# Performance work log

Hardware: AMD Instinct MI355X
Metric: run time of the kernel (lower is better)

Reference implementation:

```python
import jax, jax.numpy as jnp
import numpy as np

V, K, D, T, B, M = 32000, 32, 256, 128, 128, 16
NEG = -1e9


def setup_inputs():
    key = jax.random.key(0)
    ks = jax.random.split(key, 32)
    def rn(k, shape):
        return (0.05 * jax.random.normal(k, shape)).astype(jnp.float32)
    u = jax.random.uniform(ks[4], (T, B, K), minval=1e-6, maxval=1.0 - 1e-6)
    return dict(
        keys=jax.random.randint(ks[0], (B, M), 1, V),
        vals=jax.random.randint(ks[1], (B, M), 1, V),
        sentences=jax.random.randint(ks[2], (B, T), 1, V),
        sent_lens=jax.random.randint(ks[3], (B,), T // 2, T + 1),
        tau=jnp.float32(0.5),
        x_lambd=jnp.float32(0.5),
        gumbel_noise=(-jnp.log(-jnp.log(u))).astype(jnp.float32),
        drop_unif=jax.random.uniform(ks[5], (B, T)).astype(jnp.float32),
        emb=rn(ks[6], (V, D)), z_emb=rn(ks[7], (K, D)),
        enc_Wih=rn(ks[8], (D, 4 * D)), enc_Whh=rn(ks[9], (D, 4 * D)), enc_b=jnp.zeros((4 * D,), jnp.float32),
        crf_W=rn(ks[10], (D, K)), crf_b=jnp.zeros((K,), jnp.float32), crf_trans=rn(ks[11], (K, K)),
        init_Wh=rn(ks[12], (D, D)), init_bh=jnp.zeros((D,), jnp.float32),
        init_Wc=rn(ks[13], (D, D)), init_bc=jnp.zeros((D,), jnp.float32),
        dec_Wih=rn(ks[14], (D, 4 * D)), dec_Whh=rn(ks[15], (D, 4 * D)), dec_b=jnp.zeros((4 * D,), jnp.float32),
        attn_Wq=rn(ks[16], (D, D)), attn_Wk=rn(ks[17], (D, D)), attn_v=rn(ks[18], (D,)),
        attn_out_W=rn(ks[19], (2 * D, D)), attn_out_b=jnp.zeros((D,), jnp.float32),
        pz_W=rn(ks[20], (D, K)), pz_b=jnp.zeros((K,), jnp.float32),
        int_W=rn(ks[21], (2 * D, D)), int_b=jnp.zeros((D,), jnp.float32),
        out_W=rn(ks[22], (D, V)), out_b=jnp.zeros((V,), jnp.float32),
        cattn_Wq=rn(ks[23], (D, D)), cattn_Wk=rn(ks[24], (D, D)), cattn_v=rn(ks[25], (D,)),
        g_W=rn(ks[26], (D, 1)), g_b=jnp.zeros((1,), jnp.float32),
    )


def _lstm_step(h, c, x, Wih, Whh, b):
    g = x @ Wih + h @ Whh + b
    i, f, gg, o = jnp.split(g, 4, axis=-1)
    c = jax.nn.sigmoid(f) * c + jax.nn.sigmoid(i) * jnp.tanh(gg)
    h = jax.nn.sigmoid(o) * jnp.tanh(c)
    return h, c


def _attend(q, memk, mem_vals, mask, v):
    # additive attention: q [B,D], memk = mem @ Wk [B,M,D]
    e = jnp.einsum('bmd,d->bm', jnp.tanh(q[:, None, :] + memk), v)
    e = jnp.where(mask, e, NEG)
    a = jax.nn.softmax(e, axis=-1)
    ctx = jnp.einsum('bm,bmd->bd', a, mem_vals)
    return ctx, a


def _forward(tau, x_lambd, gumbel_noise, drop_unif, emb, z_emb,
             enc_Wih, enc_Whh, enc_b, crf_W, crf_b, crf_trans,
             init_Wh, init_bh, init_Wc, init_bc,
             dec_Wih, dec_Whh, dec_b,
             attn_Wq, attn_Wk, attn_v, attn_out_W, attn_out_b,
             pz_W, pz_b, int_W, int_b, out_W, out_b,
             cattn_Wq, cattn_Wk, cattn_v, g_W, g_b,
             keys, vals, sentences, sent_lens):
    z_beta = 1.0
    lens = sent_lens
    # ---- q encoder: 1-layer LSTM over sentence embeddings ----
    sent_emb = emb[sentences]                            # [B,T,D]
    def enc_step(carry, x_t):
        h, c = _lstm_step(carry[0], carry[1], x_t, enc_Wih, enc_Whh, enc_b)
        return (h, c), h
    z0 = jnp.zeros((B, D), jnp.float32)
    _, enc_out = jax.lax.scan(enc_step, (z0, z0), sent_emb.transpose(1, 0, 2))
    enc_out = enc_out.transpose(1, 0, 2)                 # [B,T,D]
    # ---- emission scores with overlap logits ----
    phi = enc_out @ crf_W + crf_b                        # [B,T,K]
    phi = phi.at[:, :-1].add(phi[:, 1:])                 # scores[:,:-1] += scores[:,1:].clone()
    phi = phi.at[:, 1:].add(phi[:, :-1])                 # scores[:,1:]  += scores[:,:-1].clone()
    # ---- linear-chain CRF forward recursion: alpha + exact entropy ----
    phiT = phi.transpose(1, 0, 2)                        # [T,B,K]
    def crf_step(carry, inputs):
        alpha, H = carry
        phi_t, t = inputs
        scores = alpha[:, :, None] + crf_trans[None]     # [B,Ki,Kj]
        lZ = jax.nn.logsumexp(scores, axis=1)            # [B,Kj]
        logw = scores - lZ[:, None, :]
        w = jnp.exp(logw)
        na = lZ + phi_t
        nH = jnp.sum(w * (H[:, :, None] - logw), axis=1)
        m = (t < lens)[:, None]
        na = jnp.where(m, na, alpha)
        nH = jnp.where(m, nH, H)
        return (na, nH), na
    (aT, HT), alphas = jax.lax.scan(
        crf_step, (phiT[0], jnp.zeros((B, K), jnp.float32)),
        (phiT[1:], jnp.arange(1, T)))
    alphas = jnp.concatenate([phiT[0][None], alphas], axis=0)   # [T,B,K]
    logp_last = jax.nn.log_softmax(aT, axis=-1)
    ent_z = jnp.mean(jnp.sum(jnp.exp(logp_last) * (HT - logp_last), axis=-1))
    # ---- Gumbel FFBS backward sampling ----
    def bwd_step(nid, inputs):
        alpha_t, g_t, t = inputs
        is_last = (t == lens - 1)[:, None]
        active = (t < lens)
        logits = jnp.where(is_last, alpha_t, alpha_t + crf_trans[:, nid].T)
        y = jax.nn.softmax((logits + g_t) / tau, axis=-1)
        y = jnp.where(active[:, None], y, 0.0)
        ids = jnp.where(active, jnp.argmax(y, axis=-1).astype(jnp.int32), 0)
        return ids, (ids, y)
    ts = jnp.arange(T)
    _, (ids_r, y_r) = jax.lax.scan(
        bwd_step, jnp.zeros((B,), jnp.int32),
        (alphas[::-1], gumbel_noise[::-1], ts[::-1]))
    z_ids = ids_r[::-1].transpose(1, 0)                  # [B,T]
    z_sample = y_r[::-1].transpose(1, 0, 2)              # [B,T,K]
    z_sample_emb = z_sample @ z_emb                      # soft gumbel encode [B,T,D]
    # ---- key-value table encoding ----
    kv_mask = keys != 0
    kv_emb = emb[keys] + emb[vals]                       # [B,M,D]
    kvm = kv_mask.astype(jnp.float32)
    kv_enc = (kv_emb * kvm[..., None]).sum(1) / kvm.sum(1, keepdims=True)
    # ---- decoder io (word dropout x_lambd, z[0] zeroed) ----
    zse = z_sample_emb.at[:, 0].multiply(0.0)
    wmask = (drop_unif > x_lambd).astype(jnp.float32)[..., None]
    dec_inputs = (zse + sent_emb * wmask)[:, :-1]        # [B,T-1,D]
    tgt_x = sentences[:, 1:]
    tgt_z = z_ids[:, 1:]
    z_next = z_sample_emb[:, 1:]
    h0 = kv_enc @ init_Wh + init_bh
    c0 = kv_enc @ init_Wc + init_bc
    memk = kv_emb @ attn_Wk
    memk2 = kv_emb @ cattn_Wk
    rows = jnp.arange(B)
    def dec_step(carry, inputs):
        h, c = carry
        x_t, zn_t, tx, tz = inputs
        h, c = _lstm_step(h, c, x_t, dec_Wih, dec_Whh, dec_b)
        ctx, _ = _attend(h @ attn_Wq, memk, kv_emb, kv_mask, attn_v)
        dec_out = jnp.concatenate([h, ctx], axis=-1) @ attn_out_W + attn_out_b
        z_logits = dec_out @ pz_W + pz_b
        lpz = jnp.take_along_axis(jax.nn.log_softmax(z_logits, -1), tz[:, None], 1)[:, 0]
        dec_int = jnp.concatenate([dec_out, zn_t], axis=-1) @ int_W + int_b
        lm_prob = jax.nn.softmax(dec_int @ out_W + out_b, axis=-1)       # [B,V]
        _, copy_dist = _attend(dec_int @ cattn_Wq, memk2, kv_emb, kv_mask, cattn_v)
        copy_prob = jnp.zeros((B, V), lm_prob.dtype).at[rows[:, None], keys].add(copy_dist)
        g = jax.nn.sigmoid(dec_int @ g_W + g_b)                           # [B,1]
        out_prob = (1.0 - g) * lm_prob + g * copy_prob
        lpx = jnp.log(jnp.take_along_axis(out_prob, tx[:, None], 1)[:, 0] + 1e-10)
        return (h, c), (lpx, lpz)
    _, (lpx, lpz) = jax.lax.scan(
        dec_step, (h0, c0),
        (dec_inputs.transpose(1, 0, 2), z_next.transpose(1, 0, 2),
         tgt_x.transpose(1, 0), tgt_z.transpose(1, 0)))
    steps = jnp.arange(T - 1)
    smask = (steps[None, :] < lens[:, None]).astype(jnp.float32)
    denom = jnp.sum(lens).astype(jnp.float32)
    p_log_prob = (jnp.sum(lpx.transpose(1, 0) * smask) + jnp.sum(lpz.transpose(1, 0) * smask)) / denom
    loss = -(z_beta * ent_z + p_log_prob)
    return loss


def reference(keys, vals, sentences, sent_lens, tau, x_lambd, gumbel_noise,
              drop_unif, emb, z_emb, enc_Wih, enc_Whh, enc_b, crf_W, crf_b,
              crf_trans, init_Wh, init_bh, init_Wc, init_bc, dec_Wih, dec_Whh,
              dec_b, attn_Wq, attn_Wk, attn_v, attn_out_W, attn_out_b, pz_W,
              pz_b, int_W, int_b, out_W, out_b, cattn_Wq, cattn_Wk, cattn_v,
              g_W, g_b):
    return _forward(tau, x_lambd, gumbel_noise, drop_unif, emb, z_emb,
                    enc_Wih, enc_Whh, enc_b, crf_W, crf_b, crf_trans,
                    init_Wh, init_bh, init_Wc, init_bc, dec_Wih, dec_Whh,
                    dec_b, attn_Wq, attn_Wk, attn_v, attn_out_W, attn_out_b,
                    pz_W, pz_b, int_W, int_b, out_W, out_b,
                    cattn_Wq, cattn_Wk, cattn_v, g_W, g_b,
                    keys, vals, sentences, sent_lens)
```

## Files before the change

### kernel.cpp

```cpp
#include <hip/hip_runtime.h>
#include <math.h>

namespace {

constexpr int V_  = 32000;
constexpr int K_  = 32;
constexpr int D_  = 256;
constexpr int T_  = 128;
constexpr int B_  = 128;
constexpr int M_  = 16;
constexpr int D4_ = 1024;
constexpr int TD_ = T_ - 1;
constexpr int R_  = B_ * TD_;
constexpr int NCH_ = 8;

typedef __attribute__((ext_vector_type(8))) short short8;
typedef __attribute__((ext_vector_type(4))) float f32x4;
typedef __attribute__((ext_vector_type(2))) float f32x2;

__device__ __forceinline__ float d_rcp(float x){
#if __has_builtin(__builtin_amdgcn_rcpf)
  return __builtin_amdgcn_rcpf(x);
#else
  return 1.0f / x;
#endif
}
__device__ __forceinline__ float d_sig(float x){
  return d_rcp(1.0f + __expf(-x));
}
__device__ __forceinline__ float d_tanh(float x){
  float e = __expf(2.0f*x);
  return 1.0f - 2.0f*d_rcp(e + 1.0f);
}
__device__ __forceinline__ unsigned short f2bf(float f){
  unsigned int x = __float_as_uint(f);
  unsigned int r = (x + 0x7FFFu + ((x>>16)&1u)) >> 16;
  return (unsigned short)r;
}

__device__ __forceinline__ unsigned f2fp8(float f){
  unsigned u = __float_as_uint(f);
  unsigned s = (u>>31)<<7;
  float a = fabsf(f);
  if (a < 0.015625f){
    int m = (int)rintf(a*512.0f);
    if (m >= 8) return s | 0x08u;
    return s | (unsigned)m;
  }
  unsigned t = u & 0x7FFFFFFFu;
  t += 0x7FFFFu + ((t>>20)&1u);
  int E = (int)(t>>23) - 127 + 7;
  if (E >= 16) return s | 0x7Eu;
  return s | ((unsigned)E<<3) | ((t>>20)&7u);
}

__device__ __forceinline__ unsigned pack4_fp8(float a, float b, float c, float d){
#if __has_builtin(__builtin_amdgcn_cvt_pk_fp8_f32)
  unsigned r = (unsigned)__builtin_amdgcn_cvt_pk_fp8_f32(a, b, 0, false);
  r = (unsigned)__builtin_amdgcn_cvt_pk_fp8_f32(c, d, (int)r, true);
  return r;
#else
  return f2fp8(a) | (f2fp8(b)<<8) | (f2fp8(c)<<16) | (f2fp8(d)<<24);
#endif
}
__device__ __forceinline__ unsigned char f2fp8_b(float f){
#if __has_builtin(__builtin_amdgcn_cvt_pk_fp8_f32)
  return (unsigned char)(__builtin_amdgcn_cvt_pk_fp8_f32(f, f, 0, false) & 0xFF);
#else
  return (unsigned char)f2fp8(f);
#endif
}

__device__ __forceinline__ void cvt4_fp8(unsigned w, float* o){
#if __has_builtin(__builtin_amdgcn_cvt_pk_f32_fp8)
  f32x2 lo = __builtin_amdgcn_cvt_pk_f32_fp8(w, false);
  f32x2 hi = __builtin_amdgcn_cvt_pk_f32_fp8(w, true);
  o[0]=lo.x; o[1]=lo.y; o[2]=hi.x; o[3]=hi.y;
#else
  #pragma unroll
  for (int j = 0; j < 4; j++){
    unsigned b = (w>>(8*j)) & 0xFFu;
    unsigned e = (b>>3) & 15u, m = b & 7u;
    float mag = e ? __uint_as_float(((e+120u)<<23)|(m<<20)) : (float)m*0.001953125f;
    o[j] = (b & 0x80u) ? -mag : mag;
  }
#endif
}

__global__ void k_emb2(const int* __restrict__ sent, const int* __restrict__ keys,
                       const int* __restrict__ vals, const float* __restrict__ emb,
                       float* __restrict__ sent_emb, float* __restrict__ kv){
  int bid = blockIdx.x, tid = threadIdx.x;
  if (bid < B_*T_){
    sent_emb[(size_t)bid*256 + tid] = emb[(size_t)sent[bid]*D_ + tid];
  } else {
    int r = bid - B_*T_;
    kv[(size_t)r*256 + tid] = emb[(size_t)keys[r]*D_ + tid]
                            + emb[(size_t)vals[r]*D_ + tid];
  }
}

__global__ void k_kv_enc(const int* __restrict__ keys, const float* __restrict__ kv,
                         float* __restrict__ out){
  int idx = blockIdx.x*256 + threadIdx.x;
  int b = idx >> 8, d = idx & 255;
  float s = 0.0f, c = 0.0f;
  for (int m = 0; m < M_; m++){
    if (keys[b*M_+m] != 0){ s += kv[(size_t)(b*M_+m)*D_ + d]; c += 1.0f; }
  }
  out[idx] = s / c;
}

__global__ void k_rowgemm(const float* __restrict__ A, const float* __restrict__ W,
                          const float* __restrict__ bias, float* __restrict__ C,
                          int inner, int cols){
  __shared__ float sA[256];
  int r = blockIdx.x;
  if ((int)threadIdx.x < inner) sA[threadIdx.x] = A[(size_t)r*inner + threadIdx.x];
  __syncthreads();
  for (int j = threadIdx.x; j < cols; j += blockDim.x){
    float acc = bias ? bias[j] : 0.0f;
    #pragma unroll 4
    for (int d = 0; d < inner; d++) acc += sA[d]*W[(size_t)d*cols + j];
    C[(size_t)r*cols + j] = acc;
  }
}

__global__ void k_rowgemm2(const float* __restrict__ A,
                           const float* __restrict__ W1, const float* __restrict__ b1,
                           float* __restrict__ C1,
                           const float* __restrict__ W2, const float* __restrict__ b2,
                           float* __restrict__ C2, int inner, int cols){
  __shared__ float sA[256];
  int r = blockIdx.x;
  if ((int)threadIdx.x < inner) sA[threadIdx.x] = A[(size_t)r*inner + threadIdx.x];
  __syncthreads();
  for (int j = threadIdx.x; j < cols; j += blockDim.x){
    float a1 = b1 ? b1[j] : 0.0f;
    float a2 = b2 ? b2[j] : 0.0f;
    #pragma unroll 4
    for (int d = 0; d < inner; d++){
      float a = sA[d];
      a1 += a*W1[(size_t)d*cols + j];
      a2 += a*W2[(size_t)d*cols + j];
    }
    C1[(size_t)r*cols + j] = a1;
    C2[(size_t)r*cols + j] = a2;
  }
}

__global__ __launch_bounds__(256) void k_wt8(const float* __restrict__ W,
                                             unsigned char* __restrict__ Wt8, int ldw){
  __shared__ unsigned char st[64][272];
  int tid = threadIdx.x; size_t c0 = (size_t)blockIdx.x*64;
  for (int l = tid; l < 64*256; l += 256){
    int k = l >> 6, c = l & 63;
    st[c][k] = f2fp8_b(W[(size_t)k*ldw + c0 + c]);
  }
  __syncthreads();
  for (int l = tid; l < 64*16; l += 256){
    int c = l >> 4, s = l & 15;
    *reinterpret_cast<uint4*>(&Wt8[(c0+c)*256 + s*16]) =
      *reinterpret_cast<const uint4*>(&st[c][s*16]);
  }
}

__global__ __launch_bounds__(256) void k_wt8_2(const float* __restrict__ W1,
    const float* __restrict__ W2, unsigned char* __restrict__ O1,
    unsigned char* __restrict__ O2, int ldw){
  __shared__ unsigned char st[64][272];
  const float* W = (blockIdx.x < 16) ? W1 : W2;
  unsigned char* O = (blockIdx.x < 16) ? O1 : O2;
  int tid = threadIdx.x; size_t c0 = (size_t)(blockIdx.x & 15)*64;
  for (int l = tid; l < 64*256; l += 256){
    int k = l >> 6, c = l & 63;
    st[c][k] = f2fp8_b(W[(size_t)k*ldw + c0 + c]);
  }
  __syncthreads();
  for (int l = tid; l < 64*16; l += 256){
    int c = l >> 4, s = l & 15;
    *reinterpret_cast<uint4*>(&O[(c0+c)*256 + s*16]) =
      *reinterpret_cast<const uint4*>(&st[c][s*16]);
  }
}

__global__ __launch_bounds__(256) void k_wtg2(const float* __restrict__ W1,
    const float* __restrict__ W2, unsigned short* __restrict__ O1,
    unsigned short* __restrict__ O2, int ldw){
  __shared__ unsigned short st[64][264];
  const float* W = (blockIdx.x < 16) ? W1 : W2;
  unsigned short* O = (blockIdx.x < 16) ? O1 : O2;
  int tid = threadIdx.x; size_t c0 = (size_t)(blockIdx.x & 15)*64;
  for (int l = tid; l < 64*256; l += 256){
    int k = l >> 6, c = l & 63;
    st[c][k] = f2bf(W[(size_t)k*ldw + c0 + c]);
  }
  __syncthreads();
  for (int l = tid; l < 64*32; l += 256){
    int c = l >> 5, s = l & 31;
    *reinterpret_cast<uint4*>(&O[(c0+c)*256 + s*8]) =
      *reinterpret_cast<const uint4*>(&st[c][s*8]);
  }
}

__global__ __launch_bounds__(256) void k_wtg6(
    const float* s0, const float* s1, const float* s2,
    const float* s3, const float* s4, const float* s5,
    unsigned short* d0, unsigned short* d1, unsigned short* d2,
    unsigned short* d3, unsigned short* d4, unsigned short* d5){
  __shared__ unsigned short st[64][264];
  int m = blockIdx.x >> 2, blk = blockIdx.x & 3;
  const float* S; unsigned short* D;
  if      (m == 0){ S = s0; D = d0; }
  else if (m == 1){ S = s1; D = d1; }
  else if (m == 2){ S = s2; D = d2; }
  else if (m == 3){ S = s3; D = d3; }
  else if (m == 4){ S = s4; D = d4; }
  else            { S = s5; D = d5; }
  int tid = threadIdx.x; size_t c0 = (size_t)blk*64;
  for (int l = tid; l < 64*256; l += 256){
    int k = l >> 6, c = l & 63;
    st[c][k] = f2bf(S[(size_t)k*256 + c0 + c]);
  }
  __syncthreads();
  for (int l = tid; l < 64*32; l += 256){
    int c = l >> 5, s = l & 31;
    *reinterpret_cast<uint4*>(&D[(c0+c)*256 + s*8]) =
      *reinterpret_cast<const uint4*>(&st[c][s*8]);
  }
}

template<int G1, int G2, int HALVES, int CPB, bool BIAS, int TMD>
__global__ __launch_bounds__(512) void k_gemm(
    const float* __restrict__ A1, const float* __restrict__ A2,
    const unsigned short* __restrict__ W1, const unsigned short* __restrict__ W2,
    const float* __restrict__ bias, float* __restrict__ C, int cols,
    const float* __restrict__ drop, const float* __restrict__ xl){
  __shared__ unsigned short Al[128*256];
  __shared__ unsigned short Wl[64*256];
  int tid = threadIdx.x;
  int row0 = blockIdx.x*128;
  int w = tid >> 6, l = tid & 63;
  int arow = 16*w + (l & 15);
  float xlv = 0.0f;
  if constexpr (G1==1) xlv = xl[0];
  f32x4 acc[CPB][4];
  #pragma unroll
  for (int cc=0;cc<CPB;cc++)
    #pragma unroll
    for (int nf=0;nf<4;nf++) acc[cc][nf] = (f32x4){0.f,0.f,0.f,0.f};

  for (int h = 0; h < HALVES; h++){
    const float* Asrc = h ? A2 : A1;
    const unsigned short* Wt = h ? W2 : W1;
    int gm = h ? G2 : G1;
    __syncthreads();
    #pragma unroll
    for (int q = 0; q < 8; q++){
      int u = tid + q*512;
      int row = u >> 5, slot = u & 31;
      int r = row0 + row;
      float vals[8];
      if (gm == 0){
        const float* s = Asrc + (size_t)r*256 + slot*8;
        #pragma unroll
        for (int j=0;j<8;j++) vals[j] = s[j];
      } else if (gm == 1){
        int b = r / TD_, t = r - b*TD_;
        int bt = b*T_ + t;
        float wm = (drop[bt] > xlv) ? 1.0f : 0.0f;
        const float* se = A1 + (size_t)bt*256 + slot*8;
        const float* zs = A2 + (size_t)bt*256 + slot*8;
        #pragma unroll
        for (int j=0;j<8;j++) vals[j] = se[j]*wm + (t>0 ? zs[j] : 0.0f);
      } else {
        int b = r / TD_, t = r - b*TD_;
        const float* s = Asrc + (size_t)(b*T_ + t + 1)*256 + slot*8;
        #pragma unroll
        for (int j=0;j<8;j++) vals[j] = s[j];
      }
      union { unsigned short us[8]; uint4 v4; } tu;
      #pragma unroll
      for (int j=0;j<8;j++) tu.us[j] = f2bf(vals[j]);
      int dst = row*512 + ((slot*16) ^ ((row&7)<<4));
      *reinterpret_cast<uint4*>(reinterpret_cast<char*>(Al) + dst) = tu.v4;
    }
    __syncthreads();
    short8 afr[8];
    #pragma unroll
    for (int k0 = 0; k0 < 8; k0++){
      int kb = k0*64 + ((l>>4)*16);
      afr[k0] = *reinterpret_cast<const short8*>(
          reinterpret_cast<const char*>(Al) + arow*512 + (kb ^ ((arow&7)<<4)));
    }
    for (int cc = 0; cc < CPB; cc++){
      int col0 = (blockIdx.y*CPB + cc)*64;
      __syncthreads();
      #pragma unroll
      for (int q = 0; q < 4; q++){
        int u = tid + q*512;
        int c = u >> 5, slot = u & 31;
        int dst = c*512 + ((slot*16) ^ ((c&7)<<4));
        *reinterpret_cast<uint4*>(reinterpret_cast<char*>(Wl) + dst) =
          *reinterpret_cast<const uint4*>(
              reinterpret_cast<const char*>(Wt) + (size_t)(col0+c)*512 + slot*16);
      }
      __syncthreads();
      #pragma unroll
      for (int k0 = 0; k0 < 8; k0++){
        int kb = k0*64 + ((l>>4)*16);
        #pragma unroll
        for (int nf = 0; nf < 4; nf++){
          int bc = nf*16 + (l & 15);
          short8 bfr = *reinterpret_cast<const short8*>(
              reinterpret_cast<const char*>(Wl) + bc*512 + (kb ^ ((bc&7)<<4)));
          acc[cc][nf] = __builtin_amdgcn_mfma_f32_16x16x32_bf16(afr[k0], bfr, acc[cc][nf], 0, 0, 0);
        }
      }
    }
  }
  #pragma unroll
  for (int cc = 0; cc < CPB; cc++){
    int col0 = (blockIdx.y*CPB + cc)*64;
    #pragma unroll
    for (int nf = 0; nf < 4; nf++){
      int col = col0 + nf*16 + (l & 15);
      float bv = BIAS ? bias[col] : 0.0f;
      #pragma unroll
      for (int r4 = 0; r4 < 4; r4++){
        int row = row0 + 16*w + (l>>4)*4 + r4;
        size_t orow;
        if constexpr (TMD == 0){
          orow = (size_t)row;
        } else {
          int bb = row / TMD, tt = row - bb*TMD;
          orow = (size_t)tt*B_ + bb;
        }
        C[orow*cols + col] = acc[cc][nf][r4] + bv;
      }
    }
  }
}

__global__ __launch_bounds__(1024, 4) void k_lstm12(
    const float* __restrict__ xW,
    const unsigned char* __restrict__ Wt,
    const float* __restrict__ h0, const float* __restrict__ c0,
    float* __restrict__ Hout,
    int NT){
  __shared__ unsigned char Wl[512*256];
  __shared__ unsigned char Ahl[2][16*256];
  int g0 = blockIdx.x;
  int tid = threadIdx.x;
  int w = tid >> 6, l = tid & 63;

  for (int i = tid; i < 512*16; i += 1024){
    int c = i >> 4, s16 = i & 15;
    int dst = c*256 + ((s16*16) ^ ((c&7)<<4));
    *reinterpret_cast<uint4*>(&Wl[dst]) =
      *reinterpret_cast<const uint4*>(&Wt[(size_t)c*256 + s16*16]);
  }
  if (tid < 256){
    int row = tid >> 4, gblk = tid & 15;
    unsigned pk[4];
    #pragma unroll
    for (int g = 0; g < 4; g++){
      float v0 = h0 ? h0[(size_t)(g0*16+row)*256 + gblk*16 + 4*g + 0] : 0.0f;
      float v1 = h0 ? h0[(size_t)(g0*16+row)*256 + gblk*16 + 4*g + 1] : 0.0f;
      float v2 = h0 ? h0[(size_t)(g0*16+row)*256 + gblk*16 + 4*g + 2] : 0.0f;
      float v3 = h0 ? h0[(size_t)(g0*16+row)*256 + gblk*16 + 4*g + 3] : 0.0f;
      pk[g] = pack4_fp8(v0, v1, v2, v3);
    }
    int dst = row*256 + ((gblk*16) ^ ((row&7)<<4));
    *reinterpret_cast<uint4*>(&Ahl[0][dst]) = *reinterpret_cast<const uint4*>(pk);
  }
  int cb = 16*w + (l & 15);
  int arow = l & 15;
  float creg[4];
  #pragma unroll
  for (int r = 0; r < 4; r++)
    creg[r] = c0 ? c0[(size_t)(g0*16 + (l>>4)*4 + r)*256 + cb] : 0.0f;

  int aoff[8], b0off[8], b1off[8];
  #pragma unroll
  for (int k0 = 0; k0 < 8; k0++){
    int kb = k0*32 + ((l>>4)*8);
    aoff[k0]  = arow*256 + (kb ^ ((arow&7)<<4));
    b0off[k0] = cb*256 + (kb ^ ((cb&7)<<4));
    b1off[k0] = (256+cb)*256 + (kb ^ ((cb&7)<<4));
  }
  const unsigned char* wg2 = Wt + (size_t)(512+cb)*256 + ((l>>4)*8);
  const unsigned char* wg3 = Wt + (size_t)(768+cb)*256 + ((l>>4)*8);
  int astore[4];
  const float* xb[4];
  float* hp[4];
  #pragma unroll
  for (int r = 0; r < 4; r++){
    int batch = (l>>4)*4 + r;
    astore[r] = batch*256 + ((cb & 0xF0) ^ ((batch&7)<<4)) + (cb & 15);
    xb[r] = xW + (size_t)(g0*16 + batch)*1024 + cb;
    hp[r] = Hout + (size_t)(g0*16 + batch)*NT*256 + cb;
  }
  __syncthreads();

  float xn[4][4];
  #pragma unroll
  for (int gt = 0; gt < 4; gt++)
    #pragma unroll
    for (int r = 0; r < 4; r++)
      xn[gt][r] = xb[r][gt*256];

  for (int t = 0; t < NT; t++){
    int cur = t & 1, nxt = cur ^ 1;
    f32x4 acc[4];
    #pragma unroll
    for (int gt = 0; gt < 4; gt++)
      #pragma unroll
      for (int r = 0; r < 4; r++)
        acc[gt][r] = xn[gt][r];
    if (t + 1 < NT){
      #pragma unroll
      for (int r = 0; r < 4; r++) xb[r] += B_*1024;
      #pragma unroll
      for (int gt = 0; gt < 4; gt++)
        #pragma unroll
        for (int r = 0; r < 4; r++)
          xn[gt][r] = xb[r][gt*256];
    }
    const unsigned char* Ac = Ahl[cur];
    #pragma unroll
    for (int k0 = 0; k0 < 8; k0++){
      long long afr = *reinterpret_cast<const long long*>(Ac + aoff[k0]);
      long long b0 = *reinterpret_cast<const long long*>(Wl + b0off[k0]);
      long long b1 = *reinterpret_cast<const long long*>(Wl + b1off[k0]);
      long long b2 = *reinterpret_cast<const long long*>(wg2 + k0*32);
      long long b3 = *reinterpret_cast<const long long*>(wg3 + k0*32);
      acc[0] = __builtin_amdgcn_mfma_f32_16x16x32_fp8_fp8(afr, b0, acc[0], 0, 0, 0);
      acc[1] = __builtin_amdgcn_mfma_f32_16x16x32_fp8_fp8(afr, b1, acc[1], 0, 0, 0);
      acc[2] = __builtin_amdgcn_mfma_f32_16x16x32_fp8_fp8(afr, b2, acc[2], 0, 0, 0);
      acc[3] = __builtin_amdgcn_mfma_f32_16x16x32_fp8_fp8(afr, b3, acc[3], 0, 0, 0);
    }
    #pragma unroll
    for (int r = 0; r < 4; r++){
      float vi = acc[0][r], vf = acc[1][r];
      float vg = acc[2][r], vo = acc[3][r];
      float cn = d_sig(vf)*creg[r] + d_sig(vi)*d_tanh(vg);
      float hn = d_sig(vo)*d_tanh(cn);
      creg[r] = cn;
      Ahl[nxt][astore[r]] = f2fp8_b(hn);
      hp[r][0] = hn;
      hp[r] += 256;
    }
    __syncthreads();
  }
}

__global__ __launch_bounds__(256) void k_phi(const float* __restrict__ H,
    const float* __restrict__ Wc, const float* __restrict__ bc,
    float* __restrict__ phi){
  __shared__ float sH[8][256];
  int tid = threadIdx.x; int rl = tid >> 5, j = tid & 31;
  int r0 = blockIdx.x*8;
  for (int i = tid; i < 512; i += 256){
    int rr = i >> 6, c4 = i & 63;
    *reinterpret_cast<float4*>(&sH[rr][c4*4]) =
      *reinterpret_cast<const float4*>(&H[(size_t)(r0+rr)*256 + c4*4]);
  }
  __syncthreads();
  int r = r0 + rl;
  int b = r >> 7, t = r & 127;
  float acc = bc[j];
  #pragma unroll 4
  for (int d = 0; d < 256; d++) acc += sH[rl][d]*Wc[d*K_ + j];
  phi[(size_t)t*B_*K_ + b*K_ + j] = acc;
}

__global__ __launch_bounds__(256) void k_zlp(const float* __restrict__ A,
    const float* __restrict__ Wz, const float* __restrict__ bz,
    const int* __restrict__ zids, float* __restrict__ lpz){
  __shared__ float sA[8][256];
  int tid = threadIdx.x; int rl = tid >> 5, j = tid & 31;
  int r0 = blockIdx.x*8;
  for (int i = tid; i < 512; i += 256){
    int rr = i >> 6, c4 = i & 63;
    *reinterpret_cast<float4*>(&sA[rr][c4*4]) =
      *reinterpret_cast<const float4*>(&A[(size_t)(r0+rr)*256 + c4*4]);
  }
  __syncthreads();
  int r = r0 + rl;
  float acc = bz[j];
  #pragma unroll 4
  for (int d = 0; d < 256; d++) acc += sA[rl][d]*Wz[d*K_ + j];
  float m = acc;
  #pragma unroll
  for (int off=16; off; off>>=1) m = fmaxf(m, __shfl_xor(m, off, 32));
  float e = __expf(acc - m), E = e;
  #pragma unroll
  for (int off=16; off; off>>=1) E += __shfl_xor(E, off, 32);
  int b = r / TD_, t = r - b*TD_;
  int tz = zids[b*T_ + t + 1];
  float vtz = __shfl(acc, tz, 32);
  if (j == 0) lpz[r] = vtz - (m + logf(E));
}

__global__ __launch_bounds__(1024) void k_crf(
    const float* __restrict__ phi, const float* __restrict__ trans,
    const int* __restrict__ lens, float* __restrict__ alphas,
    float* __restrict__ ent_b){
  __shared__ float sal[2][K_], sH[2][K_];
  int tid = threadIdx.x, b = blockIdx.x;
  int i = tid & 31, j = tid >> 5;
  float tr = trans[i*K_ + j];
  int len = lens[b];
  if (tid < K_){
    float a0 = phi[b*K_ + tid] + phi[(size_t)B_*K_ + b*K_ + tid];
    sal[0][tid] = a0; sH[0][tid] = 0.0f;
    alphas[b*K_ + tid] = a0;
  }
  __syncthreads();
  for (int t = 1; t < T_; t++){
    int cur = (t-1) & 1, nxt = t & 1;
    bool active = (t < len);
    float ai = sal[cur][i], Hi = sH[cur][i];
    float aj = sal[cur][j], Hj = sH[cur][j];
    float s = ai + tr;
    float m = s;
    #pragma unroll
    for (int off=16; off; off>>=1) m = fmaxf(m, __shfl_xor(m, off, 32));
    float e = expf(s - m);
    float E = e;
    #pragma unroll
    for (int off=16; off; off>>=1) E += __shfl_xor(E, off, 32);
    float lZ = m + logf(E);
    float w = e / E;
    float logw = s - lZ;
    float nH = w * (Hi - logw);
    #pragma unroll
    for (int off=16; off; off>>=1) nH += __shfl_xor(nH, off, 32);
    float pm = phi[(size_t)(t-1)*B_*K_ + b*K_ + j];
    float pt = phi[(size_t)t*B_*K_ + b*K_ + j];
    float ps = (t == T_-1) ? (pm + 2.0f*pt)
                           : (pm + 2.0f*pt + phi[(size_t)(t+1)*B_*K_ + b*K_ + j]);
    float na = lZ + ps;
    float outa = active ? na : aj;
    float outH = active ? nH : Hj;
    if (i == 0){
      sal[nxt][j] = outa; sH[nxt][j] = outH;
      alphas[(size_t)t*B_*K_ + b*K_ + j] = outa;
    }
    __syncthreads();
  }
  int fb = (T_-1) & 1;
  if (tid < K_){
    float a = sal[fb][tid];
    float m = a;
    #pragma unroll
    for (int off=16; off; off>>=1) m = fmaxf(m, __shfl_xor(m, off, 32));
    float e = expf(a-m), E = e;
    #pragma unroll
    for (int off=16; off; off>>=1) E += __shfl_xor(E, off, 32);
    float lse = m + logf(E);
    float lp = a - lse;
    float v = expf(lp)*(sH[fb][tid]-lp);
    #pragma unroll
    for (int off=16; off; off>>=1) v += __shfl_xor(v, off, 32);
    if (tid == 0) ent_b[b] = v;
  }
}

__global__ void k_sampler(const float* __restrict__ alphas, const float* __restrict__ trans,
                          const float* __restrict__ gum, const int* __restrict__ lens,
                          const float* __restrict__ tau_p,
                          float* __restrict__ y_all, int* __restrict__ z_ids){
  int b = blockIdx.x;
  int lane = threadIdx.x;
  int k = lane & 31;
  float inv_tau = d_rcp(tau_p[0]);
  int len = lens[b];
  int nid = 0;
  for (int t = T_-1; t >= 0; t--){
    bool active  = (t < len);
    bool is_last = (t == len-1);
    float a = alphas[(size_t)t*B_*K_ + b*K_ + k];
    float lg = is_last ? a : a + trans[k*K_ + nid];
    float val = (lg + gum[(size_t)t*B_*K_ + b*K_ + k]) * inv_tau;
    float m = val;
    #pragma unroll
    for (int off=16; off; off>>=1) m = fmaxf(m, __shfl_xor(m, off, 32));
    float e = expf(val - m), E = e;
    #pragma unroll
    for (int off=16; off; off>>=1) E += __shfl_xor(E, off, 32);
    float y = active ? e*d_rcp(E) : 0.0f;
    if (lane < K_) y_all[(size_t)(b*T_ + t)*K_ + k] = y;
    float bv = val; int bk = k;
    #pragma unroll
    for (int off=16; off; off>>=1){
      float ov = __shfl_xor(bv, off, 32);
      int   ok = __shfl_xor(bk, off, 32);
      if (ov > bv || (ov == bv && ok < bk)){ bv = ov; bk = ok; }
    }
    int ids = active ? bk : 0;
    nid = ids;
    if (lane == 0) z_ids[b*T_ + t] = ids;
  }
}

__global__ __launch_bounds__(256) void k_attn1(
    const float* __restrict__ q, const float* __restrict__ memk,
    const float* __restrict__ kv_emb, const int* __restrict__ keys,
    const float* __restrict__ av, float* __restrict__ ctx){
  __shared__ float se[16];
  int r = blockIdx.x, tid = threadIdx.x;
  int b = r / TD_;
  int m = tid >> 4, ds = tid & 15;
  float p = 0.0f;
  #pragma unroll 4
  for (int qq = 0; qq < 16; qq++){
    int dd = ds + qq*16;
    p += d_tanh(q[(size_t)r*256 + dd] + memk[(size_t)(b*M_+m)*256 + dd]) * av[dd];
  }
  #pragma unroll
  for (int off=8; off; off>>=1) p += __shfl_xor(p, off, 16);
  if (ds == 0) se[m] = (keys[b*M_+m] != 0) ? p : -1e9f;
  __syncthreads();
  float mx = -1e30f;
  #pragma unroll
  for (int mm=0;mm<16;mm++) mx = fmaxf(mx, se[mm]);
  float den = 0.0f, ex[16];
  #pragma unroll
  for (int mm=0;mm<16;mm++){ ex[mm] = __expf(se[mm]-mx); den += ex[mm]; }
  float cacc = 0.0f;
  #pragma unroll
  for (int mm=0;mm<16;mm++) cacc += ex[mm]*kv_emb[(size_t)(b*M_+mm)*256 + tid];
  ctx[(size_t)r*256 + tid] = cacc*d_rcp(den);
}

__global__ __launch_bounds__(256) void k_attn2g(
    const float* __restrict__ q2, const float* __restrict__ dint,
    const float* __restrict__ memk2, const int* __restrict__ keys,
    const float* __restrict__ cv, const float* __restrict__ gW, const float* __restrict__ gb,
    const int* __restrict__ sent,
    float* __restrict__ cpx, float* __restrict__ gsig){
  __shared__ float se2[16];
  __shared__ float sred[4];
  int r = blockIdx.x, tid = threadIdx.x;
  int b = r / TD_, t = r - b*TD_;
  int m = tid >> 4, ds = tid & 15;
  float p = 0.0f;
  #pragma unroll 4
  for (int qq = 0; qq < 16; qq++){
    int dd = ds + qq*16;
    p += d_tanh(q2[(size_t)r*256 + dd] + memk2[(size_t)(b*M_+m)*256 + dd]) * cv[dd];
  }
  #pragma unroll
  for (int off=8; off; off>>=1) p += __shfl_xor(p, off, 16);
  if (ds == 0) se2[m] = (keys[b*M_+m] != 0) ? p : -1e9f;
  float gp = dint[(size_t)r*256 + tid]*gW[tid];
  #pragma unroll
  for (int off=32; off; off>>=1) gp += __shfl_xor(gp, off, 64);
  if ((tid & 63) == 0) sred[tid>>6] = gp;
  __syncthreads();
  if (tid == 0){
    float mx = -1e30f;
    #pragma unroll
    for (int mm=0;mm<16;mm++) mx = fmaxf(mx, se2[mm]);
    float den = 0.0f, ex[16];
    #pragma unroll
    for (int mm=0;mm<16;mm++){ ex[mm] = __expf(se2[mm]-mx); den += ex[mm]; }
    int txi = sent[b*T_ + t + 1];
    float idn = d_rcp(den);
    float cp = 0.0f;
    #pragma unroll
    for (int mm=0;mm<16;mm++) if (keys[b*M_+mm] == txi) cp += ex[mm]*idn;
    cpx[r] = cp;
    gsig[r] = d_sig(sred[0]+sred[1]+sred[2]+sred[3] + gb[0]);
  }
}

__global__ void k_a8(const float* __restrict__ dint, unsigned* __restrict__ A8){
  int idx = blockIdx.x*256 + threadIdx.x;
  if (idx >= R_*64) return;
  float4 f = *reinterpret_cast<const float4*>(dint + (size_t)idx*4);
  A8[idx] = pack4_fp8(f.x, f.y, f.z, f.w);
}

__global__ __launch_bounds__(512) void k_lse8(
    const unsigned char* __restrict__ A8,
    const unsigned char* __restrict__ Wt8,
    const float* __restrict__ bias,
    float* __restrict__ part){
  __shared__ unsigned char Al[256*256];
  __shared__ unsigned char Wl[64*256];
  int tid = threadIdx.x;
  int row0 = blockIdx.x*256;
  #pragma unroll
  for (int q = 0; q < 8; q++){
    int u = tid + q*512;
    int row = u >> 4, s16 = u & 15;
    int r = row0 + row;
    uint4 pk = (uint4){0u,0u,0u,0u};
    if (r < R_)
      pk = *reinterpret_cast<const uint4*>(A8 + (size_t)r*256 + s16*16);
    int dst = row*256 + ((s16*16) ^ ((row&7)<<4));
    *reinterpret_cast<uint4*>(&Al[dst]) = pk;
  }
  __syncthreads();
  int w = tid >> 6, l = tid & 63;
  int arow = 16*w + (l & 15);
  long long afrA[8], afrB[8];
  #pragma unroll
  for (int k0 = 0; k0 < 8; k0++){
    int kb = k0*32 + ((l>>4)*8);
    afrA[k0] = *reinterpret_cast<const long long*>(&Al[arow*256 + (kb ^ ((arow&7)<<4))]);
    int ar2 = arow + 128;
    afrB[k0] = *reinterpret_cast<const long long*>(&Al[ar2*256 + (kb ^ ((ar2&7)<<4))]);
  }
  float rm[2][4], rs[2][4];
  #pragma unroll
  for (int rf=0;rf<2;rf++)
    #pragma unroll
    for (int r4=0;r4<4;r4++){ rm[rf][r4] = -3.0e38f; rs[rf][r4] = 0.0f; }

  for (int ct = blockIdx.y; ct < 500; ct += NCH_){
    int col0 = ct*64;
    __syncthreads();
    #pragma unroll
    for (int q = 0; q < 2; q++){
      int u = tid + q*512;
      int c = u >> 4, s16 = u & 15;
      int dst = c*256 + ((s16*16) ^ ((c&7)<<4));
      *reinterpret_cast<uint4*>(&Wl[dst]) =
        *reinterpret_cast<const uint4*>(&Wt8[(size_t)(col0+c)*256 + s16*16]);
    }
    __syncthreads();
    f32x4 acc[2][4];
    #pragma unroll
    for (int rf=0;rf<2;rf++)
      #pragma unroll
      for (int nf=0;nf<4;nf++) acc[rf][nf] = (f32x4){0.f,0.f,0.f,0.f};
    #pragma unroll
    for (int k0 = 0; k0 < 8; k0++){
      int kb = k0*32 + ((l>>4)*8);
      #pragma unroll
      for (int nf = 0; nf < 4; nf++){
        int bc = nf*16 + (l & 15);
        long long bfr = *reinterpret_cast<const long long*>(&Wl[bc*256 + (kb ^ ((bc&7)<<4))]);
        acc[0][nf] = __builtin_amdgcn_mfma_f32_16x16x32_fp8_fp8(afrA[k0], bfr, acc[0][nf], 0, 0, 0);
        acc[1][nf] = __builtin_amdgcn_mfma_f32_16x16x32_fp8_fp8(afrB[k0], bfr, acc[1][nf], 0, 0, 0);
      }
    }
    float bb[4];
    #pragma unroll
    for (int nf=0;nf<4;nf++) bb[nf] = bias[col0 + nf*16 + (l&15)];
    #pragma unroll
    for (int rf = 0; rf < 2; rf++){
      #pragma unroll
      for (int r4 = 0; r4 < 4; r4++){
        float v0 = acc[rf][0][r4]+bb[0], v1 = acc[rf][1][r4]+bb[1];
        float v2 = acc[rf][2][r4]+bb[2], v3 = acc[rf][3][r4]+bb[3];
        float tm = fmaxf(fmaxf(v0,v1), fmaxf(v2,v3));
        float ts = __expf(v0-tm)+__expf(v1-tm)+__expf(v2-tm)+__expf(v3-tm);
        float m0 = rm[rf][r4];
        if (tm <= m0){
          rs[rf][r4] += ts*__expf(tm - m0);
        } else {
          rs[rf][r4] = rs[rf][r4]*__expf(m0 - tm) + ts;
          rm[rf][r4] = tm;
        }
      }
    }
  }
  #pragma unroll
  for (int rf = 0; rf < 2; rf++){
    #pragma unroll
    for (int r4 = 0; r4 < 4; r4++){
      float M = rm[rf][r4];
      #pragma unroll
      for (int off=8; off; off>>=1) M = fmaxf(M, __shfl_xor(M, off, 16));
      float S = rs[rf][r4]*__expf(rm[rf][r4] - M);
      #pragma unroll
      for (int off=8; off; off>>=1) S += __shfl_xor(S, off, 16);
      if ((l & 15) == 0){
        int grow = row0 + rf*128 + 16*w + (l>>4)*4 + r4;
        if (grow < R_){
          part[((size_t)grow*NCH_ + blockIdx.y)*2 + 0] = M;
          part[((size_t)grow*NCH_ + blockIdx.y)*2 + 1] = S;
        }
      }
    }
  }
}

__global__ void k_lse_combine(const float* __restrict__ part, float* __restrict__ lse){
  int r = blockIdx.x*256 + threadIdx.x;
  if (r >= R_) return;
  float M = -3.0e38f;
  for (int c = 0; c < NCH_; c++) M = fmaxf(M, part[((size_t)r*NCH_+c)*2]);
  float S = 0.0f;
  for (int c = 0; c < NCH_; c++){
    float m = part[((size_t)r*NCH_+c)*2], s = part[((size_t)r*NCH_+c)*2+1];
    S += s*__expf(m - M);
  }
  lse[r] = M + logf(S);
}

__global__ __launch_bounds__(256) void k_ltx(const unsigned char* __restrict__ A8,
    const unsigned char* __restrict__ Wt8, const float* __restrict__ bias,
    const int* __restrict__ sent, float* __restrict__ out){
  int tid = threadIdx.x;
  int r = blockIdx.x*4 + (tid >> 6);
  int lane = tid & 63;
  int b = r / TD_, t = r - b*TD_;
  int tx = sent[b*T_ + t + 1];
  unsigned wq = *reinterpret_cast<const unsigned*>(Wt8 + (size_t)tx*256 + lane*4);
  float wv[4]; cvt4_fp8(wq, wv);
  unsigned aq = *reinterpret_cast<const unsigned*>(A8 + (size_t)r*256 + lane*4);
  float av[4]; cvt4_fp8(aq, av);
  float acc = av[0]*wv[0] + av[1]*wv[1] + av[2]*wv[2] + av[3]*wv[3];
  #pragma unroll
  for (int off=32; off; off>>=1) acc += __shfl_xor(acc, off, 64);
  if (lane == 0) out[r] = acc + bias[tx];
}

__global__ __launch_bounds__(256) void k_final(
    const float* __restrict__ lse, const float* __restrict__ ltx,
    const float* __restrict__ gsig, const float* __restrict__ cpx,
    const float* __restrict__ lpz, const float* __restrict__ ent_b,
    const int* __restrict__ lens, float* __restrict__ out){
  __shared__ float sred[256];
  int tid = threadIdx.x;
  float sum = 0.0f;
  for (int r = tid; r < R_; r += 256){
    int b = r / TD_, t = r % TD_;
    if (t < lens[b]){
      float g = gsig[r];
      float lm = __expf(ltx[r] - lse[r]);
      float p = (1.0f-g)*lm + g*cpx[r] + 1e-10f;
      sum += logf(p) + lpz[r];
    }
  }
  sred[tid] = sum;
  __syncthreads();
  for (int s = 128; s; s >>= 1){ if (tid < s) sred[tid] += sred[tid+s]; __syncthreads(); }
  if (tid == 0){
    float es = 0.0f, dn = 0.0f;
    for (int b = 0; b < B_; b++){ es += ent_b[b]; dn += (float)lens[b]; }
    out[0] = -( es/(float)B_ + sred[0]/dn );
  }
}

}

extern "C" void kernel_launch(void* const* d_in, const int* in_sizes, int n_in,
                              void* d_out, int out_size, void* d_ws, size_t ws_size,
                              hipStream_t stream){
  const int*   keys  = (const int*)d_in[0];
  const int*   vals  = (const int*)d_in[1];
  const int*   sent  = (const int*)d_in[2];
  const int*   lens  = (const int*)d_in[3];
  const float* tau   = (const float*)d_in[4];
  const float* xl    = (const float*)d_in[5];
  const float* gum   = (const float*)d_in[6];
  const float* drop  = (const float*)d_in[7];
  const float* emb   = (const float*)d_in[8];
  const float* z_emb = (const float*)d_in[9];
  const float* eWih  = (const float*)d_in[10];
  const float* eWhh  = (const float*)d_in[11];
  const float* eb    = (const float*)d_in[12];
  const float* crfW  = (const float*)d_in[13];
  const float* crfb  = (const float*)d_in[14];
  const float* trans = (const float*)d_in[15];
  const float* iWh   = (const float*)d_in[16];
  const float* ibh   = (const float*)d_in[17];
  const float* iWc   = (const float*)d_in[18];
  const float* ibc   = (const float*)d_in[19];
  const float* dWih  = (const float*)d_in[20];
  const float* dWhh  = (const float*)d_in[21];
  const float* db    = (const float*)d_in[22];
  const float* aWq   = (const float*)d_in[23];
  const float* aWk   = (const float*)d_in[24];
  const float* av    = (const float*)d_in[25];
  const float* aoW   = (const float*)d_in[26];
  const float* aob   = (const float*)d_in[27];
  const float* pzW   = (const float*)d_in[28];
  const float* pzb   = (const float*)d_in[29];
  const float* intW  = (const float*)d_in[30];
  const float* intb  = (const float*)d_in[31];
  const float* outW  = (const float*)d_in[32];
  const float* outb  = (const float*)d_in[33];
  const float* cWq   = (const float*)d_in[34];
  const float* cWk   = (const float*)d_in[35];
  const float* cv    = (const float*)d_in[36];
  const float* gW    = (const float*)d_in[37];
  const float* gb    = (const float*)d_in[38];
  (void)in_sizes; (void)n_in; (void)out_size; (void)ws_size;

  float* ws = (float*)d_ws;
  size_t o = 0;
  auto alloc = [&](size_t n){ size_t r = o; o += (n + 3) & ~(size_t)3; return r; };
  float* sent_emb = ws + alloc((size_t)B_*T_*D_);
  float* kv_emb   = ws + alloc((size_t)B_*M_*D_);
  float* kv_enc   = ws + alloc((size_t)B_*D_);
  float* h0       = ws + alloc((size_t)B_*D_);
  float* c0       = ws + alloc((size_t)B_*D_);
  float* memk     = ws + alloc((size_t)B_*M_*D_);
  float* memk2    = ws + alloc((size_t)B_*M_*D_);
  float* xW       = ws + alloc((size_t)B_*T_*D4_);
  float* encH     = ws + alloc((size_t)B_*T_*D_);
  float* phi_raw  = ws + alloc((size_t)T_*B_*K_);
  float* alphas   = ws + alloc((size_t)T_*B_*K_);
  float* ent_b    = ws + alloc((size_t)B_);
  float* y_all    = ws + alloc((size_t)B_*T_*K_);
  float* zse      = ws + alloc((size_t)B_*T_*D_);
  float* qbuf     = ws + alloc((size_t)R_*D_);
  float* ctx      = ws + alloc((size_t)R_*D_);
  float* dec_out  = ws + alloc((size_t)R_*D_);
  float* dint     = ws + alloc((size_t)R_*D_);
  float* lpz_b    = ws + alloc((size_t)R_);
  float* gsig     = ws + alloc((size_t)R_);
  float* cpx      = ws + alloc((size_t)R_);
  float* ltx      = ws + alloc((size_t)R_);
  float* lse      = ws + alloc((size_t)R_);
  float* part     = ws + alloc((size_t)R_*NCH_*2);
  int*   z_ids    = (int*)(ws + alloc((size_t)B_*T_));
  unsigned* A8    = (unsigned*)(ws + alloc((size_t)R_*64));
  unsigned char* WhhT8E = (unsigned char*)(ws + alloc((size_t)D4_*D_/4));
  unsigned char* WhhT8D = (unsigned char*)(ws + alloc((size_t)D4_*D_/4));
  unsigned char* Wt8    = (unsigned char*)(ws + alloc((size_t)V_*D_/4));
  unsigned short* eWihT = (unsigned short*)(ws + alloc((size_t)D4_*D_/2));
  unsigned short* dWihT = (unsigned short*)(ws + alloc((size_t)D4_*D_/2));
  unsigned short* aWqT  = (unsigned short*)(ws + alloc((size_t)D_*D_/2));
  unsigned short* cWqT  = (unsigned short*)(ws + alloc((size_t)D_*D_/2));
  unsigned short* aoWtT = (unsigned short*)(ws + alloc((size_t)D_*D_/2));
  unsigned short* aoWbT = (unsigned short*)(ws + alloc((size_t)D_*D_/2));
  unsigned short* inWtT = (unsigned short*)(ws + alloc((size_t)D_*D_/2));
  unsigned short* inWbT = (unsigned short*)(ws + alloc((size_t)D_*D_/2));

  float* Hdec = encH;

  k_emb2<<<B_*T_ + B_*M_, 256, 0, stream>>>(sent, keys, vals, emb, sent_emb, kv_emb);
  k_kv_enc<<<B_*D_/256, 256, 0, stream>>>(keys, kv_emb, kv_enc);
  k_rowgemm2<<<B_, 256, 0, stream>>>(kv_enc, iWh, ibh, h0, iWc, ibc, c0, 256, 256);
  k_rowgemm2<<<B_*M_, 256, 0, stream>>>(kv_emb, aWk, nullptr, memk,
                                        cWk, nullptr, memk2, 256, 256);
  k_wt8_2<<<32, 256, 0, stream>>>(eWhh, dWhh, WhhT8E, WhhT8D, D4_);
  k_wt8<<<V_/64, 256, 0, stream>>>(outW, Wt8, V_);
  k_wtg2<<<32, 256, 0, stream>>>(eWih, dWih, eWihT, dWihT, D4_);
  k_wtg6<<<24, 256, 0, stream>>>(aWq, cWq, aoW, aoW + 256*256, intW, intW + 256*256,
                                 aWqT, cWqT, aoWtT, aoWbT, inWtT, inWbT);

  k_gemm<0,0,1,4,true,T_><<<dim3(B_*T_/128, 4), 512, 0, stream>>>(
      sent_emb, nullptr, eWihT, nullptr, eb, xW, D4_, nullptr, nullptr);
  k_lstm12<<<B_/16, 1024, 0, stream>>>(xW, WhhT8E, nullptr, nullptr, encH, T_);
  k_phi<<<B_*T_/8, 256, 0, stream>>>(encH, crfW, crfb, phi_raw);
  k_crf<<<B_, 1024, 0, stream>>>(phi_raw, trans, lens, alphas, ent_b);
  k_sampler<<<B_, 64, 0, stream>>>(alphas, trans, gum, lens, tau, y_all, z_ids);
  k_rowgemm<<<B_*T_, 256, 0, stream>>>(y_all, z_emb, nullptr, zse, K_, 256);

  k_gemm<1,0,1,4,true,TD_><<<dim3(R_/128, 4), 512, 0, stream>>>(
      sent_emb, zse, dWihT, nullptr, db, xW, D4_, drop, xl);
  k_lstm12<<<B_/16, 1024, 0, stream>>>(xW, WhhT8D, h0, c0, Hdec, TD_);

  k_gemm<0,0,1,1,false,0><<<dim3(R_/128, 4), 512, 0, stream>>>(
      Hdec, nullptr, aWqT, nullptr, nullptr, qbuf, D_, nullptr, nullptr);
  k_attn1<<<R_, 256, 0, stream>>>(qbuf, memk, kv_emb, keys, av, ctx);
  k_gemm<0,0,2,1,true,0><<<dim3(R_/128, 4), 512, 0, stream>>>(
      Hdec, ctx, aoWtT, aoWbT, aob, dec_out, D_, nullptr, nullptr);
  k_zlp<<<R_/8, 256, 0, stream>>>(dec_out, pzW, pzb, z_ids, lpz_b);
  k_gemm<0,2,2,1,true,0><<<dim3(R_/128, 4), 512, 0, stream>>>(
      dec_out, zse, inWtT, inWbT, intb, dint, D_, nullptr, nullptr);
  k_a8<<<(R_*64+255)/256, 256, 0, stream>>>(dint, A8);
  k_gemm<0,0,1,1,false,0><<<dim3(R_/128, 4), 512, 0, stream>>>(
      dint, nullptr, cWqT, nullptr, nullptr, qbuf, D_, nullptr, nullptr);
  k_attn2g<<<R_, 256, 0, stream>>>(qbuf, dint, memk2, keys, cv, gW, gb, sent,
                                   cpx, gsig);

  k_lse8<<<dim3((R_+255)/256, NCH_), 512, 0, stream>>>(
      (const unsigned char*)A8, Wt8, outb, part);
  k_lse_combine<<<(R_+255)/256, 256, 0, stream>>>(part, lse);
  k_ltx<<<R_/4, 256, 0, stream>>>((const unsigned char*)A8, Wt8, outb, sent, ltx);
  k_final<<<1, 256, 0, stream>>>(lse, ltx, gsig, cpx, lpz_b, ent_b, lens, (float*)d_out);
}
```

Baseline: 1.712 ms.

## Double-buffer vocab weight tiles and halve row tile in fp8 LSE kernel

```diff
diff --git a/kernel.cpp b/kernel.cpp
--- a/kernel.cpp
+++ b/kernel.cpp
@@ -689,103 +689,110 @@
     const unsigned char* __restrict__ Wt8,
     const float* __restrict__ bias,
     float* __restrict__ part){
-  __shared__ unsigned char Al[256*256];
-  __shared__ unsigned char Wl[64*256];
+  __shared__ unsigned char Al[128*256];
+  __shared__ unsigned char Wl[2][64*256];
   int tid = threadIdx.x;
-  int row0 = blockIdx.x*256;
-  #pragma unroll
-  for (int q = 0; q < 8; q++){
+  int row0 = blockIdx.x*128;
+  #pragma unroll
+  for (int q = 0; q < 4; q++){
     int u = tid + q*512;
-    int row = u >> 4, s16 = u & 15;
+    int row = u >> 4, s16a = u & 15;
     int r = row0 + row;
     uint4 pk = (uint4){0u,0u,0u,0u};
     if (r < R_)
-      pk = *reinterpret_cast<const uint4*>(A8 + (size_t)r*256 + s16*16);
-    int dst = row*256 + ((s16*16) ^ ((row&7)<<4));
+      pk = *reinterpret_cast<const uint4*>(A8 + (size_t)r*256 + s16a*16);
+    int dst = row*256 + ((s16a*16) ^ ((row&7)<<4));
     *reinterpret_cast<uint4*>(&Al[dst]) = pk;
   }
-  __syncthreads();
+  int s16 = tid & 15;
+  int c0q = tid >> 4;
+  int c1q = c0q + 32;
+  int src0 = c0q*256 + s16*16;
+  int src1 = c1q*256 + s16*16;
+  int dst0 = c0q*256 + ((s16*16) ^ ((c0q&7)<<4));
+  int dst1 = c1q*256 + ((s16*16) ^ ((c1q&7)<<4));
+  uint4 wr0, wr1;
+  int ct0 = blockIdx.y;
+  wr0 = *reinterpret_cast<const uint4*>(Wt8 + (size_t)ct0*16384 + src0);
+  wr1 = *reinterpret_cast<const uint4*>(Wt8 + (size_t)ct0*16384 + src1);
+  *reinterpret_cast<uint4*>(&Wl[0][dst0]) = wr0;
+  *reinterpret_cast<uint4*>(&Wl[0][dst1]) = wr1;
+  if (ct0 + NCH_ < 500){
+    wr0 = *reinterpret_cast<const uint4*>(Wt8 + (size_t)(ct0+NCH_)*16384 + src0);
+    wr1 = *reinterpret_cast<const uint4*>(Wt8 + (size_t)(ct0+NCH_)*16384 + src1);
+  }
+  __syncthreads();
+
   int w = tid >> 6, l = tid & 63;
   int arow = 16*w + (l & 15);
-  long long afrA[8], afrB[8];
+  long long afr[8];
   #pragma unroll
   for (int k0 = 0; k0 < 8; k0++){
     int kb = k0*32 + ((l>>4)*8);
-    afrA[k0] = *reinterpret_cast<const long long*>(&Al[arow*256 + (kb ^ ((arow&7)<<4))]);
-    int ar2 = arow + 128;
-    afrB[k0] = *reinterpret_cast<const long long*>(&Al[ar2*256 + (kb ^ ((ar2&7)<<4))]);
-  }
-  float rm[2][4], rs[2][4];
-  #pragma unroll
-  for (int rf=0;rf<2;rf++)
-    #pragma unroll
-    for (int r4=0;r4<4;r4++){ rm[rf][r4] = -3.0e38f; rs[rf][r4] = 0.0f; }
-
-  for (int ct = blockIdx.y; ct < 500; ct += NCH_){
-    int col0 = ct*64;
-    __syncthreads();
-    #pragma unroll
-    for (int q = 0; q < 2; q++){
-      int u = tid + q*512;
-      int c = u >> 4, s16 = u & 15;
-      int dst = c*256 + ((s16*16) ^ ((c&7)<<4));
-      *reinterpret_cast<uint4*>(&Wl[dst]) =
-        *reinterpret_cast<const uint4*>(&Wt8[(size_t)(col0+c)*256 + s16*16]);
-    }
-    __syncthreads();
-    f32x4 acc[2][4];
-    #pragma unroll
-    for (int rf=0;rf<2;rf++)
-      #pragma unroll
-      for (int nf=0;nf<4;nf++) acc[rf][nf] = (f32x4){0.f,0.f,0.f,0.f};
+    afr[k0] = *reinterpret_cast<const long long*>(&Al[arow*256 + (kb ^ ((arow&7)<<4))]);
+  }
+  float rm[4], rs[4];
+  #pragma unroll
+  for (int r4=0;r4<4;r4++){ rm[r4] = -3.0e38f; rs[r4] = 0.0f; }
+
+  int it = 0;
+  for (int ct = ct0; ct < 500; ct += NCH_, it++){
+    int cur = it & 1, nxt = cur ^ 1;
+    if (ct + NCH_ < 500){
+      *reinterpret_cast<uint4*>(&Wl[nxt][dst0]) = wr0;
+      *reinterpret_cast<uint4*>(&Wl[nxt][dst1]) = wr1;
+    }
+    if (ct + 2*NCH_ < 500){
+      wr0 = *reinterpret_cast<const uint4*>(Wt8 + (size_t)(ct+2*NCH_)*16384 + src0);
+      wr1 = *reinterpret_cast<const uint4*>(Wt8 + (size_t)(ct+2*NCH_)*16384 + src1);
+    }
+    const unsigned char* Wc = Wl[cur];
+    f32x4 acc[4];
+    #pragma unroll
+    for (int nf=0;nf<4;nf++) acc[nf] = (f32x4){0.f,0.f,0.f,0.f};
     #pragma unroll
     for (int k0 = 0; k0 < 8; k0++){
       int kb = k0*32 + ((l>>4)*8);
       #pragma unroll
       for (int nf = 0; nf < 4; nf++){
         int bc = nf*16 + (l & 15);
-        long long bfr = *reinterpret_cast<const long long*>(&Wl[bc*256 + (kb ^ ((bc&7)<<4))]);
-        acc[0][nf] = __builtin_amdgcn_mfma_f32_16x16x32_fp8_fp8(afrA[k0], bfr, acc[0][nf], 0, 0, 0);
-        acc[1][nf] = __builtin_amdgcn_mfma_f32_16x16x32_fp8_fp8(afrB[k0], bfr, acc[1][nf], 0, 0, 0);
+        long long bfr = *reinterpret_cast<const long long*>(&Wc[bc*256 + (kb ^ ((bc&7)<<4))]);
+        acc[nf] = __builtin_amdgcn_mfma_f32_16x16x32_fp8_fp8(afr[k0], bfr, acc[nf], 0, 0, 0);
       }
     }
+    int col0 = ct*64;
     float bb[4];
     #pragma unroll
     for (int nf=0;nf<4;nf++) bb[nf] = bias[col0 + nf*16 + (l&15)];
     #pragma unroll
-    for (int rf = 0; rf < 2; rf++){
-      #pragma unroll
-      for (int r4 = 0; r4 < 4; r4++){
-        float v0 = acc[rf][0][r4]+bb[0], v1 = acc[rf][1][r4]+bb[1];
-        float v2 = acc[rf][2][r4]+bb[2], v3 = acc[rf][3][r4]+bb[3];
-        float tm = fmaxf(fmaxf(v0,v1), fmaxf(v2,v3));
-        float ts = __expf(v0-tm)+__expf(v1-tm)+__expf(v2-tm)+__expf(v3-tm);
-        float m0 = rm[rf][r4];
-        if (tm <= m0){
-          rs[rf][r4] += ts*__expf(tm - m0);
-        } else {
-          rs[rf][r4] = rs[rf][r4]*__expf(m0 - tm) + ts;
-          rm[rf][r4] = tm;
-        }
+    for (int r4 = 0; r4 < 4; r4++){
+      float v0 = acc[0][r4]+bb[0], v1 = acc[1][r4]+bb[1];
+      float v2 = acc[2][r4]+bb[2], v3 = acc[3][r4]+bb[3];
+      float tm = fmaxf(fmaxf(v0,v1), fmaxf(v2,v3));
+      float ts = __expf(v0-tm)+__expf(v1-tm)+__expf(v2-tm)+__expf(v3-tm);
+      float m0 = rm[r4];
+      if (tm <= m0){
+        rs[r4] += ts*__expf(tm - m0);
+      } else {
+        rs[r4] = rs[r4]*__expf(m0 - tm) + ts;
+        rm[r4] = tm;
       }
     }
-  }
-  #pragma unroll
-  for (int rf = 0; rf < 2; rf++){
-    #pragma unroll
-    for (int r4 = 0; r4 < 4; r4++){
-      float M = rm[rf][r4];
-      #pragma unroll
-      for (int off=8; off; off>>=1) M = fmaxf(M, __shfl_xor(M, off, 16));
-      float S = rs[rf][r4]*__expf(rm[rf][r4] - M);
-      #pragma unroll
-      for (int off=8; off; off>>=1) S += __shfl_xor(S, off, 16);
-      if ((l & 15) == 0){
-        int grow = row0 + rf*128 + 16*w + (l>>4)*4 + r4;
-        if (grow < R_){
-          part[((size_t)grow*NCH_ + blockIdx.y)*2 + 0] = M;
-          part[((size_t)grow*NCH_ + blockIdx.y)*2 + 1] = S;
-        }
+    __syncthreads();
+  }
+  #pragma unroll
+  for (int r4 = 0; r4 < 4; r4++){
+    float M = rm[r4];
+    #pragma unroll
+    for (int off=8; off; off>>=1) M = fmaxf(M, __shfl_xor(M, off, 16));
+    float S = rs[r4]*__expf(rm[r4] - M);
+    #pragma unroll
+    for (int off=8; off; off>>=1) S += __shfl_xor(S, off, 16);
+    if ((l & 15) == 0){
+      int grow = row0 + 16*w + (l>>4)*4 + r4;
+      if (grow < R_){
+        part[((size_t)grow*NCH_ + blockIdx.y)*2 + 0] = M;
+        part[((size_t)grow*NCH_ + blockIdx.y)*2 + 1] = S;
       }
     }
   }
@@ -975,7 +982,7 @@
   k_attn2g<<<R_, 256, 0, stream>>>(qbuf, dint, memk2, keys, cv, gW, gb, sent,
                                    cpx, gsig);
 
-  k_lse8<<<dim3((R_+255)/256, NCH_), 512, 0, stream>>>(
+  k_lse8<<<dim3(R_/128, NCH_), 512, 0, stream>>>(
       (const unsigned char*)A8, Wt8, outb, part);
   k_lse_combine<<<(R_+255)/256, 256, 0, stream>>>(part, lse);
   k_ltx<<<R_/4, 256, 0, stream>>>((const unsigned char*)A8, Wt8, outb, sent, ltx);
```

Result: slower. 1.802 ms (+5.2%).
